# Optimization experiments

Hardware: AMD Instinct MI355X
Metric: run time of the kernel (lower is better)

The kernel has to match this reference:

```python
import jax, jax.numpy as jnp
import numpy as np

B, S, D, H, L, DFF, WIN = 2, 2048, 768, 12, 2, 3072, 512
EPS = 1e-5
DH = D // H


def setup_inputs() -> dict:
    key = jax.random.key(0)
    ks = jax.random.split(key, 8)
    rn = lambda k, shape: jax.random.normal(k, shape, jnp.float32) * 0.02
    inp = {
        "src": jax.random.normal(ks[0], (B, S, D), jnp.float32),
        "qw": rn(ks[1], (L, D, D)), "qb": jnp.zeros((L, D), jnp.float32),
        "kw": rn(ks[2], (L, D, D)), "kb": jnp.zeros((L, D), jnp.float32),
        "vw": rn(ks[3], (L, D, D)), "vb": jnp.zeros((L, D), jnp.float32),
        "ow": rn(ks[4], (L, D, D)), "ob": jnp.zeros((L, D), jnp.float32),
        "w1": rn(ks[5], (L, DFF, D)), "b1": jnp.zeros((L, DFF), jnp.float32),
        "w2": rn(ks[6], (L, D, DFF)), "b2": jnp.zeros((L, D), jnp.float32),
        "g1": jnp.ones((L, D), jnp.float32), "be1": jnp.zeros((L, D), jnp.float32),
        "g2": jnp.ones((L, D), jnp.float32), "be2": jnp.zeros((L, D), jnp.float32),
    }
    return inp


def _ln(x, g, b):
    m = jnp.mean(x, axis=-1, keepdims=True)
    v = jnp.mean(jnp.square(x - m), axis=-1, keepdims=True)
    return (x - m) * jax.lax.rsqrt(v + EPS) * g + b


def _encoder(src, qw, qb, kw, kb, vw, vb, ow, ob, w1, b1, w2, b2, g1, be1, g2, be2):
    scale = DH ** -0.5
    idx = jnp.arange(S)
    # non-causal sliding window: |i - j| <= window_size // 2
    band = jnp.abs(idx[:, None] - idx[None, :]) <= (WIN // 2)
    neg = -jnp.finfo(jnp.float32).max
    x = src
    for l in range(L):
        # projections -> (B, H, S, DH)
        q = (x @ qw[l].T + qb[l]).reshape(B, S, H, DH).transpose(0, 2, 1, 3)
        k = (x @ kw[l].T + kb[l]).reshape(B, S, H, DH).transpose(0, 2, 1, 3)
        v = (x @ vw[l].T + vb[l]).reshape(B, S, H, DH).transpose(0, 2, 1, 3)
        # full dense scores then band mask (faithful to the original module)
        sim = jnp.einsum('bhid,bhjd->bhij', q * scale, k)
        sim = jnp.where(band, sim, neg)
        attn = jax.nn.softmax(sim, axis=-1)
        o = jnp.einsum('bhij,bhjd->bhid', attn, v)
        o = o.transpose(0, 2, 1, 3).reshape(B, S, D) @ ow[l].T + ob[l]
        # post-norm transformer block (norm_first=False)
        x = _ln(x + o, g1[l], be1[l])
        ff = jax.nn.relu(x @ w1[l].T + b1[l]) @ w2[l].T + b2[l]
        x = _ln(x + ff, g2[l], be2[l])
    return x


def reference(src, qw, qb, kw, kb, vw, vb, ow, ob, w1, b1, w2, b2, g1, be1, g2, be2):
    return _encoder(src, qw, qb, kw, kb, vw, vb, ow, ob, w1, b1, w2, b2, g1, be1, g2, be2)
```

## Files before the change

### kernel.cpp

```cpp
#include <hip/hip_runtime.h>
#include <math.h>

#define BATCH 2
#define SEQ   2048
#define DM    768
#define NHD   12
#define NL    2
#define DFF   3072
#define DH    64
#define HW    256
#define MR    (BATCH*SEQ)
#define EPSF  1e-5f
#define SCALE 0.125f
#define QKVS  2304

typedef __attribute__((ext_vector_type(8))) __bf16 bf16x8;
typedef __attribute__((ext_vector_type(4))) float  f32x4;

__device__ __forceinline__ ushort f2bu(float f) {
    union { __bf16 h; ushort u; } c;
    c.h = (__bf16)f;
    return c.u;
}
__device__ __forceinline__ float bu2f(ushort u) {
    union { uint u; float f; } c;
    c.u = ((uint)u) << 16;
    return c.f;
}

__device__ __forceinline__ void gload16(const ushort* g, ushort* l) {
    __builtin_amdgcn_global_load_lds(
        (const __attribute__((address_space(1))) void*)g,
        (__attribute__((address_space(3))) void*)l, 16, 0, 0);
}

__device__ __forceinline__ void xcd_swz(int& bx, int& by, int& bz) {
    const int gx = gridDim.x, gy = gridDim.y;
    const int nwg = gx * gy * gridDim.z;
    int lin = bx + gx * (by + gy * bz);
    lin = (lin & 7) * (nwg >> 3) + (lin >> 3);
    bx = lin % gx;
    int rest = lin / gx;
    by = rest % gy;
    bz = rest / gy;
}

__global__ __launch_bounds__(256) void prep(
    const float* __restrict__ qw, const float* __restrict__ kw,
    const float* __restrict__ vw, const float* __restrict__ ow,
    const float* __restrict__ w1, const float* __restrict__ w2,
    const float* __restrict__ src,
    const float* __restrict__ qb, const float* __restrict__ kb,
    const float* __restrict__ vb,
    ushort* __restrict__ qkvwB, ushort* __restrict__ owB,
    ushort* __restrict__ w1B, ushort* __restrict__ w2B,
    ushort* __restrict__ xb, float* __restrict__ bcat)
{
    const int WD1C  = DM * DM;
    const int WQKVC = 3 * WD1C;
    const int WF1C  = DFF * DM;
    const int NB0 = NL * WQKVC / 1024;
    const int NB1 = NL * WD1C / 1024;
    const int NB2 = NL * WF1C / 1024;
    const int NB4 = MR * DM / 1024;

    int b = blockIdx.x;
    const int tid = threadIdx.x;

    if (b < NB0) {
        int e = b * 1024 + tid * 4;
        int l = e / WQKVC;
        int r = e % WQKVC;
        const float* s; int off;
        if (r < WD1C)          { s = qw + (size_t)l * WD1C; off = r; }
        else if (r < 2 * WD1C) { s = kw + (size_t)l * WD1C; off = r - WD1C; }
        else                   { s = vw + (size_t)l * WD1C; off = r - 2 * WD1C; }
        float4 v = *(const float4*)(s + off);
        ushort4 o4;
        o4.x = f2bu(v.x); o4.y = f2bu(v.y); o4.z = f2bu(v.z); o4.w = f2bu(v.w);
        *(ushort4*)(qkvwB + (size_t)l * WQKVC + r) = o4;
        return;
    }
    b -= NB0;
    if (b < NB1) {
        int i = b * 1024 + tid * 4;
        float4 v = *(const float4*)(ow + i);
        ushort4 o4;
        o4.x = f2bu(v.x); o4.y = f2bu(v.y); o4.z = f2bu(v.z); o4.w = f2bu(v.w);
        *(ushort4*)(owB + i) = o4;
        return;
    }
    b -= NB1;
    if (b < NB2) {
        int i = b * 1024 + tid * 4;
        float4 v = *(const float4*)(w1 + i);
        ushort4 o4;
        o4.x = f2bu(v.x); o4.y = f2bu(v.y); o4.z = f2bu(v.z); o4.w = f2bu(v.w);
        *(ushort4*)(w1B + i) = o4;
        return;
    }
    b -= NB2;
    if (b < NB2) {
        int i = b * 1024 + tid * 4;
        float4 v = *(const float4*)(w2 + i);
        ushort4 o4;
        o4.x = f2bu(v.x); o4.y = f2bu(v.y); o4.z = f2bu(v.z); o4.w = f2bu(v.w);
        *(ushort4*)(w2B + i) = o4;
        return;
    }
    b -= NB2;
    if (b < NB4) {
        int i = b * 1024 + tid * 4;
        float4 v = *(const float4*)(src + i);
        ushort4 o4;
        o4.x = f2bu(v.x); o4.y = f2bu(v.y); o4.z = f2bu(v.z); o4.w = f2bu(v.w);
        *(ushort4*)(xb + i) = o4;
        return;
    }
#pragma unroll
    for (int e = 0; e < 18; ++e) {
        int j = tid + 256 * e;
        int l = j / (3 * DM);
        int r = j % (3 * DM);
        int sel = r / DM, off = r % DM;
        const float* s = (sel == 0) ? qb : (sel == 1) ? kb : vb;
        bcat[(size_t)l * QKVS + sel * DM + off] = s[(size_t)l * DM + off];
    }
}

#define STAGE128(bi, kt) do {                                           \
        const int _k0 = (kt) * 32;                                      \
        gload16(ag + _k0,                    &As[bi][t * 8]);           \
        gload16(ag + (size_t)64 * ldk + _k0, &As[bi][2048 + t * 8]);    \
        gload16(wg + _k0,                    &Ws[bi][t * 8]);           \
        gload16(wg + (size_t)64 * ldk + _k0, &Ws[bi][2048 + t * 8]);    \
    } while (0)

__global__ __launch_bounds__(256) void gemm128(
    const ushort* __restrict__ A, const ushort* __restrict__ W,
    const float* __restrict__ bias, ushort* __restrict__ C,
    float* __restrict__ part, int M, int N, int Kc, int ldk, int relu)
{
    __shared__ ushort As[3][128 * 32];
    __shared__ ushort Ws[3][128 * 32];

    int bxi = blockIdx.x, byi = blockIdx.y, bzi = blockIdx.z;
    xcd_swz(bxi, byi, bzi);

    const int t  = threadIdx.x;
    const int bm = byi * 128;
    const int bn = bxi * 128;
    const int z  = bzi;
    const int kbase = z * Kc;

    const int w    = t >> 6;
    const int lane = t & 63;
    const int quad = lane >> 4;
    const int lrow = lane & 15;
    const int wm   = (w >> 1) * 64;
    const int wn   = (w & 1) * 64;
    const int rx   = (lrow >> 1) & 3;
    const int rq   = (quad ^ rx) * 8;

    const int srow = t >> 2;
    const int scol = (((t & 3) ^ ((t >> 3) & 3)) * 8);
    const ushort* ag = A + (size_t)(bm + srow) * ldk + kbase + scol;
    const ushort* wg = W + (size_t)(bn + srow) * ldk + kbase + scol;

    f32x4 acc[4][4] = {};
    const int NT = Kc / 32;

    STAGE128(0, 0);
    STAGE128(1, 1);

    for (int kt = 0; kt < NT; ++kt) {
        if (kt + 1 < NT)
            asm volatile("s_waitcnt vmcnt(4)" ::: "memory");
        else
            asm volatile("s_waitcnt vmcnt(0)" ::: "memory");
        __builtin_amdgcn_s_barrier();

        const int cb = kt % 3;
        bf16x8 af[4], bfr[4];
#pragma unroll
        for (int i = 0; i < 4; ++i)
            af[i] = *(const bf16x8*)&As[cb][(wm + i * 16 + lrow) * 32 + rq];
#pragma unroll
        for (int j = 0; j < 4; ++j)
            bfr[j] = *(const bf16x8*)&Ws[cb][(wn + j * 16 + lrow) * 32 + rq];

        __builtin_amdgcn_s_setprio(1);
#pragma unroll
        for (int i = 0; i < 4; ++i)
#pragma unroll
            for (int j = 0; j < 4; ++j)
                acc[i][j] = __builtin_amdgcn_mfma_f32_16x16x32_bf16(
                    af[i], bfr[j], acc[i][j], 0, 0, 0);
        __builtin_amdgcn_s_setprio(0);

        if (kt + 2 < NT) {
            const int sb = (kt + 2) % 3;
            STAGE128(sb, kt + 2);
        }
    }

    if (gridDim.z > 1) {
        float* po = part + (size_t)z * M * N;
#pragma unroll
        for (int j = 0; j < 4; ++j) {
            const int col = bn + wn + j * 16 + lrow;
#pragma unroll
            for (int i = 0; i < 4; ++i) {
                const int rb = bm + wm + i * 16 + quad * 4;
#pragma unroll
                for (int r = 0; r < 4; ++r)
                    po[(size_t)(rb + r) * N + col] = acc[i][j][r];
            }
        }
    } else {
#pragma unroll
        for (int j = 0; j < 4; ++j) {
            const int col = bn + wn + j * 16 + lrow;
            const float bv = bias[col];
#pragma unroll
            for (int i = 0; i < 4; ++i) {
                const int rb = bm + wm + i * 16 + quad * 4;
#pragma unroll
                for (int r = 0; r < 4; ++r) {
                    float vv = acc[i][j][r] + bv;
                    if (relu) vv = fmaxf(vv, 0.f);
                    C[(size_t)(rb + r) * N + col] = f2bu(vv);
                }
            }
        }
    }
}

#define STAGE64(bi, kt) do {                                            \
        const int _k0 = (kt) * 32;                                      \
        gload16(ag + _k0,                    &As[bi][t * 8]);           \
        gload16(wg + _k0,                    &Ws[bi][t * 8]);           \
        gload16(wg + (size_t)64 * ldk + _k0, &Ws[bi][2048 + t * 8]);    \
    } while (0)

__global__ __launch_bounds__(256) void gemm64(
    const ushort* __restrict__ A, const ushort* __restrict__ W,
    const float* __restrict__ bias, ushort* __restrict__ C,
    float* __restrict__ part, int M, int N, int Kc, int ldk, int relu)
{
    __shared__ ushort As[3][64 * 32];
    __shared__ ushort Ws[3][128 * 32];

    int bxi = blockIdx.x, byi = blockIdx.y, bzi = blockIdx.z;
    xcd_swz(bxi, byi, bzi);

    const int t  = threadIdx.x;
    const int bm = byi * 64;
    const int bn = bxi * 128;
    const int z  = bzi;
    const int kbase = z * Kc;

    const int w    = t >> 6;
    const int lane = t & 63;
    const int quad = lane >> 4;
    const int lrow = lane & 15;
    const int wm   = (w >> 1) * 32;
    const int wn   = (w & 1) * 64;
    const int rx   = (lrow >> 1) & 3;
    const int rq   = (quad ^ rx) * 8;

    const int srow = t >> 2;
    const int scol = (((t & 3) ^ ((t >> 3) & 3)) * 8);
    const ushort* ag = A + (size_t)(bm + srow) * ldk + kbase + scol;
    const ushort* wg = W + (size_t)(bn + srow) * ldk + kbase + scol;

    f32x4 acc[2][4] = {};
    const int NT = Kc / 32;

    STAGE64(0, 0);
    STAGE64(1, 1);

    for (int kt = 0; kt < NT; ++kt) {
        if (kt + 1 < NT)
            asm volatile("s_waitcnt vmcnt(3)" ::: "memory");
        else
            asm volatile("s_waitcnt vmcnt(0)" ::: "memory");
        __builtin_amdgcn_s_barrier();

        const int cb = kt % 3;
        bf16x8 af[2], bfr[4];
#pragma unroll
        for (int i = 0; i < 2; ++i)
            af[i] = *(const bf16x8*)&As[cb][(wm + i * 16 + lrow) * 32 + rq];
#pragma unroll
        for (int j = 0; j < 4; ++j)
            bfr[j] = *(const bf16x8*)&Ws[cb][(wn + j * 16 + lrow) * 32 + rq];

        __builtin_amdgcn_s_setprio(1);
#pragma unroll
        for (int i = 0; i < 2; ++i)
#pragma unroll
            for (int j = 0; j < 4; ++j)
                acc[i][j] = __builtin_amdgcn_mfma_f32_16x16x32_bf16(
                    af[i], bfr[j], acc[i][j], 0, 0, 0);
        __builtin_amdgcn_s_setprio(0);

        if (kt + 2 < NT) {
            const int sb = (kt + 2) % 3;
            STAGE64(sb, kt + 2);
        }
    }

    if (gridDim.z > 1) {
        float* po = part + (size_t)z * M * N;
#pragma unroll
        for (int j = 0; j < 4; ++j) {
            const int col = bn + wn + j * 16 + lrow;
#pragma unroll
            for (int i = 0; i < 2; ++i) {
                const int rb = bm + wm + i * 16 + quad * 4;
#pragma unroll
                for (int r = 0; r < 4; ++r)
                    po[(size_t)(rb + r) * N + col] = acc[i][j][r];
            }
        }
    } else {
#pragma unroll
        for (int j = 0; j < 4; ++j) {
            const int col = bn + wn + j * 16 + lrow;
            const float bv = bias[col];
#pragma unroll
            for (int i = 0; i < 2; ++i) {
                const int rb = bm + wm + i * 16 + quad * 4;
#pragma unroll
                for (int r = 0; r < 4; ++r) {
                    float vv = acc[i][j][r] + bv;
                    if (relu) vv = fmaxf(vv, 0.f);
                    C[(size_t)(rb + r) * N + col] = f2bu(vv);
                }
            }
        }
    }
}

#define QT  128
#define NCH 10
#define KP  72

__global__ __launch_bounds__(512) void attn(
    const ushort* __restrict__ q, const ushort* __restrict__ k,
    const ushort* __restrict__ v, ushort* __restrict__ o)
{
    __shared__ ushort kv[2][64][KP];
    __shared__ ushort vt[2][64][KP];
    __shared__ ushort sc[QT][KP];

    int bxi = blockIdx.x, byi = blockIdx.y, bzi = blockIdx.z;
    xcd_swz(bxi, byi, bzi);

    const int t    = threadIdx.x;
    const int i0   = bxi * QT;
    const int h    = byi;
    const int b    = bzi;
    const size_t ibase = (size_t)b * SEQ * QKVS + (size_t)h * DH;
    const size_t obase = (size_t)b * SEQ * DM   + (size_t)h * DH;

    const int w    = t >> 6;
    const int lane = t & 63;
    const int quad = lane >> 4;
    const int lrow = lane & 15;
    const int qrow = w * 16;

    const int jstart = i0 - HW;
    const int clo = (qrow + 78) >> 6;
    const int chi = (qrow + 449) >> 6;

    const int sjj = t >> 3;
    const int sd0 = (t & 7) * 8;

#pragma unroll
    for (int e = 0; e < 2; ++e) {
        int idx = t + 512 * e;
        int qi = idx >> 3, d0 = (idx & 7) * 8;
        uint4 raw = *(const uint4*)(q + ibase + (size_t)(i0 + qi) * QKVS + d0);
        *(uint4*)&sc[qi][d0] = raw;
    }
    uint4 kr, vr;
    {
        int j = jstart + sjj;
        kr = make_uint4(0, 0, 0, 0);
        vr = make_uint4(0, 0, 0, 0);
        if (j >= 0 && j < SEQ) {
            kr = *(const uint4*)(k + ibase + (size_t)j * QKVS + sd0);
            vr = *(const uint4*)(v + ibase + (size_t)j * QKVS + sd0);
        }
    }
    *(uint4*)&kv[0][sjj][sd0] = kr;
    {
        const ushort* u = (const ushort*)&vr;
#pragma unroll
        for (int x = 0; x < 8; ++x) {
            int dh  = sd0 + x;
            int blk = ((sjj >> 3) ^ (dh >> 3)) & 7;
            vt[0][dh][blk * 8 + (sjj & 7)] = u[x];
        }
    }
    __syncthreads();

    const bf16x8 a0 = *(const bf16x8*)&sc[qrow + lrow][quad * 8];
    const bf16x8 a1 = *(const bf16x8*)&sc[qrow + lrow][32 + quad * 8];

    float m_s = -1e20f, l_s = 0.f;
    f32x4 oacc[4] = {};

    for (int c = 0; c < NCH; ++c) {
        const int cur = c & 1;
        const int j0  = jstart + c * 64;

        if (c + 1 < NCH) {
            int j = jstart + (c + 1) * 64 + sjj;
            kr = make_uint4(0, 0, 0, 0);
            vr = make_uint4(0, 0, 0, 0);
            if (j >= 0 && j < SEQ) {
                kr = *(const uint4*)(k + ibase + (size_t)j * QKVS + sd0);
                vr = *(const uint4*)(v + ibase + (size_t)j * QKVS + sd0);
            }
        }

        const bool full = (c >= clo) && (c <= chi) &&
                          (j0 >= 0) && (j0 + 64 <= SEQ);
        float p[4][4];
#pragma unroll
        for (int kt = 0; kt < 4; ++kt) {
            const int krow = kt * 16;
            bf16x8 kf0 = *(const bf16x8*)&kv[cur][krow + lrow][quad * 8];
            bf16x8 kf1 = *(const bf16x8*)&kv[cur][krow + lrow][32 + quad * 8];
            f32x4 acc = {};
            __builtin_amdgcn_s_setprio(1);
            acc = __builtin_amdgcn_mfma_f32_16x16x32_bf16(kf0, a0, acc, 0, 0, 0);
            acc = __builtin_amdgcn_mfma_f32_16x16x32_bf16(kf1, a1, acc, 0, 0, 0);
            __builtin_amdgcn_s_setprio(0);
            if (full) {
#pragma unroll
                for (int r = 0; r < 4; ++r) p[kt][r] = acc[r] * SCALE;
            } else {
                const int ig = i0 + qrow + lrow;
#pragma unroll
                for (int r = 0; r < 4; ++r) {
                    const int jg = j0 + krow + quad * 4 + r;
                    bool ok = (jg >= 0) && (jg < SEQ) &&
                              (jg >= ig - HW) && (jg <= ig + HW);
                    p[kt][r] = ok ? acc[r] * SCALE : -1e30f;
                }
            }
        }

        float cm = p[0][0];
#pragma unroll
        for (int kt = 0; kt < 4; ++kt)
#pragma unroll
            for (int r = 0; r < 4; ++r) cm = fmaxf(cm, p[kt][r]);
        cm = fmaxf(cm, __shfl_xor(cm, 16));
        cm = fmaxf(cm, __shfl_xor(cm, 32));

        const bool resc = !__all(cm <= m_s + 8.f);
        float f = 1.f;
        if (resc) {
            const float mn = fmaxf(m_s, cm);
            f = __expf(m_s - mn);
            m_s = mn;
        }
        float cs = 0.f;
#pragma unroll
        for (int kt = 0; kt < 4; ++kt)
#pragma unroll
            for (int r = 0; r < 4; ++r) {
                float e = __expf(p[kt][r] - m_s);
                p[kt][r] = e;
                cs += e;
            }
        cs += __shfl_xor(cs, 16);
        cs += __shfl_xor(cs, 32);
        l_s = l_s * f + cs;
        if (resc) {
            float f4[4];
#pragma unroll
            for (int r = 0; r < 4; ++r) f4[r] = __shfl(f, quad * 4 + r);
#pragma unroll
            for (int nt = 0; nt < 4; ++nt)
#pragma unroll
                for (int r = 0; r < 4; ++r) oacc[nt][r] *= f4[r];
        }

#pragma unroll
        for (int kt = 0; kt < 4; ++kt) {
            ushort4 pw;
            pw.x = f2bu(p[kt][0]);
            pw.y = f2bu(p[kt][1]);
            pw.z = f2bu(p[kt][2]);
            pw.w = f2bu(p[kt][3]);
            *(ushort4*)&sc[qrow + lrow][kt * 16 + quad * 4] = pw;
        }

        bf16x8 pa0 = *(const bf16x8*)&sc[qrow + lrow][quad * 8];
        bf16x8 pa1 = *(const bf16x8*)&sc[qrow + lrow][32 + quad * 8];
        __builtin_amdgcn_s_setprio(1);
#pragma unroll
        for (int nt = 0; nt < 4; ++nt) {
            const int dh  = nt * 16 + lrow;
            const int rsw = (dh >> 3) & 7;
            bf16x8 b0 = *(const bf16x8*)&vt[cur][dh][((quad)     ^ rsw) * 8];
            bf16x8 b1 = *(const bf16x8*)&vt[cur][dh][((quad + 4) ^ rsw) * 8];
            oacc[nt] = __builtin_amdgcn_mfma_f32_16x16x32_bf16(pa0, b0, oacc[nt], 0, 0, 0);
            oacc[nt] = __builtin_amdgcn_mfma_f32_16x16x32_bf16(pa1, b1, oacc[nt], 0, 0, 0);
        }
        __builtin_amdgcn_s_setprio(0);

        if (c + 1 < NCH) {
            const int nxt = cur ^ 1;
            *(uint4*)&kv[nxt][sjj][sd0] = kr;
            const ushort* u = (const ushort*)&vr;
#pragma unroll
            for (int x = 0; x < 8; ++x) {
                int dh  = sd0 + x;
                int blk = ((sjj >> 3) ^ (dh >> 3)) & 7;
                vt[nxt][dh][blk * 8 + (sjj & 7)] = u[x];
            }
        }
        __syncthreads();
    }

    const float inv = 1.f / l_s;
    float inv4[4];
#pragma unroll
    for (int r = 0; r < 4; ++r) inv4[r] = __shfl(inv, quad * 4 + r);
#pragma unroll
    for (int r = 0; r < 4; ++r) {
        const int qi = i0 + qrow + quad * 4 + r;
#pragma unroll
        for (int nt = 0; nt < 4; ++nt)
            o[obase + (size_t)qi * DM + nt * 16 + lrow] = f2bu(oacc[nt][r] * inv4[r]);
    }
}

__global__ __launch_bounds__(256) void add_ln_sk(
    const ushort* __restrict__ xa, const float* __restrict__ pp,
    const float* __restrict__ bias, const float* __restrict__ g,
    const float* __restrict__ be,
    ushort* __restrict__ ob, float* __restrict__ of, int fin)
{
    const int r = blockIdx.x * 4 + (threadIdx.x >> 6);
    const int t = threadIdx.x & 63;
    const size_t off = (size_t)r * DM;
    const size_t pl  = (size_t)MR * DM;
    float sv[12];
    float s1 = 0.f, s2 = 0.f;
#pragma unroll
    for (int ii = 0; ii < 12; ++ii) {
        const int c = t + 64 * ii;
        float vv = bu2f(xa[off + c]) + pp[off + c] + pp[pl + off + c] + bias[c];
        sv[ii] = vv; s1 += vv; s2 += vv * vv;
    }
#pragma unroll
    for (int o2 = 32; o2; o2 >>= 1) {
        s1 += __shfl_xor(s1, o2);
        s2 += __shfl_xor(s2, o2);
    }
    const float mean = s1 * (1.f / 768.f);
    const float rstd = rsqrtf(s2 * (1.f / 768.f) - mean * mean + EPSF);
#pragma unroll
    for (int ii = 0; ii < 12; ++ii) {
        const int c = t + 64 * ii;
        float v = (sv[ii] - mean) * rstd * g[c] + be[c];
        if (fin) of[off + c] = v;
        else     ob[off + c] = f2bu(v);
    }
}

__global__ __launch_bounds__(256) void add_ln_sk3(
    const ushort* __restrict__ xa, const float* __restrict__ pp,
    const float* __restrict__ bias, const float* __restrict__ g,
    const float* __restrict__ be,
    ushort* __restrict__ ob, float* __restrict__ of, int fin)
{
    const int r = blockIdx.x * 4 + (threadIdx.x >> 6);
    const int t = threadIdx.x & 63;
    const size_t off = (size_t)r * DM;
    const size_t pl  = (size_t)MR * DM;
    float sv[12];
    float s1 = 0.f, s2 = 0.f;
#pragma unroll
    for (int ii = 0; ii < 12; ++ii) {
        const int c = t + 64 * ii;
        float vv = bu2f(xa[off + c]) + pp[off + c] + pp[pl + off + c]
                 + pp[2 * pl + off + c] + bias[c];
        sv[ii] = vv; s1 += vv; s2 += vv * vv;
    }
#pragma unroll
    for (int o2 = 32; o2; o2 >>= 1) {
        s1 += __shfl_xor(s1, o2);
        s2 += __shfl_xor(s2, o2);
    }
    const float mean = s1 * (1.f / 768.f);
    const float rstd = rsqrtf(s2 * (1.f / 768.f) - mean * mean + EPSF);
#pragma unroll
    for (int ii = 0; ii < 12; ++ii) {
        const int c = t + 64 * ii;
        float v = (sv[ii] - mean) * rstd * g[c] + be[c];
        if (fin) of[off + c] = v;
        else     ob[off + c] = f2bu(v);
    }
}

extern "C" void kernel_launch(void* const* d_in, const int* in_sizes, int n_in,
                              void* d_out, int out_size, void* d_ws, size_t ws_size,
                              hipStream_t stream) {
    (void)in_sizes; (void)n_in; (void)out_size; (void)ws_size;
    const float* src = (const float*)d_in[0];
    const float* qw  = (const float*)d_in[1];
    const float* qb  = (const float*)d_in[2];
    const float* kw  = (const float*)d_in[3];
    const float* kb  = (const float*)d_in[4];
    const float* vw  = (const float*)d_in[5];
    const float* vb  = (const float*)d_in[6];
    const float* ow  = (const float*)d_in[7];
    const float* ob  = (const float*)d_in[8];
    const float* w1  = (const float*)d_in[9];
    const float* b1  = (const float*)d_in[10];
    const float* w2  = (const float*)d_in[11];
    const float* b2  = (const float*)d_in[12];
    const float* g1  = (const float*)d_in[13];
    const float* be1 = (const float*)d_in[14];
    const float* g2  = (const float*)d_in[15];
    const float* be2 = (const float*)d_in[16];

    const size_t A    = (size_t)MR * DM;
    const size_t WD1  = (size_t)DM * DM;
    const size_t WQKV = (size_t)3 * DM * DM;
    const size_t WF1  = (size_t)DFF * DM;
    const size_t WF   = (size_t)NL * WF1;

    float*  bcat = (float*)d_ws;
    ushort* p    = (ushort*)(bcat + (size_t)NL * QKVS);
    ushort* qkvwB = p; p += (size_t)NL * WQKV;
    ushort* owB   = p; p += (size_t)NL * WD1;
    ushort* w1B   = p; p += WF;
    ushort* w2B   = p; p += WF;
    ushort* xb    = p; p += A;
    ushort* qkvB  = p; p += 3 * A;
    ushort* oB    = p; p += A;
    ushort* yB    = p; p += A;
    ushort* h1    = p; p += A;
    ushort* ffh   = p; p += 4 * A;
    ushort* x2    = p;

    float* partF = (float*)xb;
    float* partO = (float*)ffh;

    const int PB = (int)((NL * WQKV + NL * WD1 + 2 * WF + A) / 1024) + 1;
    prep<<<PB, 256, 0, stream>>>(qw, kw, vw, ow, w1, w2, src,
                                 qb, kb, vb,
                                 qkvwB, owB, w1B, w2B, xb, bcat);

    const dim3 gQKV(QKVS / 128, MR / 128);
    const dim3 gOp(DM / 128, MR / 64, 2);
    const dim3 gF1(DFF / 128, MR / 128);
    const dim3 gF2(DM / 128, MR / 128, 3);
    const dim3 gA(SEQ / QT, NHD, BATCH);

    for (int l = 0; l < NL; ++l) {
        const size_t bD = (size_t)l * DM;
        const size_t bF = (size_t)l * DFF;
        const ushort* xin = (l == 0) ? xb : x2;

        gemm128<<<gQKV, 256, 0, stream>>>(xin, qkvwB + (size_t)l * WQKV,
                                          bcat + (size_t)l * QKVS, qkvB,
                                          nullptr, MR, QKVS, DM, DM, 0);
        attn<<<gA, 512, 0, stream>>>(qkvB, qkvB + DM, qkvB + 2 * DM, oB);
        gemm64<<<gOp, 256, 0, stream>>>(oB, owB + (size_t)l * WD1, nullptr,
                                        nullptr, partO, MR, DM, DM / 2, DM, 0);
        add_ln_sk<<<MR / 4, 256, 0, stream>>>(xin, partO, ob + bD,
                                              g1 + bD, be1 + bD,
                                              h1, nullptr, 0);
        gemm128<<<gF1, 256, 0, stream>>>(h1, w1B + (size_t)l * WF1, b1 + bF, ffh,
                                         nullptr, MR, DFF, DM, DM, 1);
        gemm128<<<gF2, 256, 0, stream>>>(ffh, w2B + (size_t)l * WF1, nullptr,
                                         nullptr, partF, MR, DM, DFF / 3, DFF, 0);
        if (l == NL - 1)
            add_ln_sk3<<<MR / 4, 256, 0, stream>>>(h1, partF, b2 + bD,
                                                   g2 + bD, be2 + bD,
                                                   nullptr, (float*)d_out, 1);
        else
            add_ln_sk3<<<MR / 4, 256, 0, stream>>>(h1, partF, b2 + bD,
                                                   g2 + bD, be2 + bD,
                                                   x2, nullptr, 0);
    }
}
```

Before: 432.3 us.

## Stage GEMM epilogue through LDS and shrink attention query tile to 64

```diff
diff --git a/kernel.cpp b/kernel.cpp
--- a/kernel.cpp
+++ b/kernel.cpp
@@ -128,12 +128,12 @@
     }
 }
 
-#define STAGE128(bi, kt) do {                                           \
-        const int _k0 = (kt) * 32;                                      \
-        gload16(ag + _k0,                    &As[bi][t * 8]);           \
-        gload16(ag + (size_t)64 * ldk + _k0, &As[bi][2048 + t * 8]);    \
-        gload16(wg + _k0,                    &Ws[bi][t * 8]);           \
-        gload16(wg + (size_t)64 * ldk + _k0, &Ws[bi][2048 + t * 8]);    \
+#define STAGE128(bi, kt) do {                                             \
+        const int _k0 = (kt) * 32;                                        \
+        gload16(ag + _k0,                    As + (bi)*4096 + t * 8);     \
+        gload16(ag + (size_t)64 * ldk + _k0, As + (bi)*4096 + 2048 + t * 8); \
+        gload16(wg + _k0,                    Ws + (bi)*4096 + t * 8);     \
+        gload16(wg + (size_t)64 * ldk + _k0, Ws + (bi)*4096 + 2048 + t * 8); \
     } while (0)
 
 __global__ __launch_bounds__(256) void gemm128(
@@ -141,8 +141,9 @@
     const float* __restrict__ bias, ushort* __restrict__ C,
     float* __restrict__ part, int M, int N, int Kc, int ldk, int relu)
 {
-    __shared__ ushort As[3][128 * 32];
-    __shared__ ushort Ws[3][128 * 32];
+    __shared__ ushort smem[24576];
+    ushort* const As = smem;
+    ushort* const Ws = smem + 12288;
 
     int bxi = blockIdx.x, byi = blockIdx.y, bzi = blockIdx.z;
     xcd_swz(bxi, byi, bzi);
@@ -184,10 +185,10 @@
         bf16x8 af[4], bfr[4];
 #pragma unroll
         for (int i = 0; i < 4; ++i)
-            af[i] = *(const bf16x8*)&As[cb][(wm + i * 16 + lrow) * 32 + rq];
+            af[i] = *(const bf16x8*)&As[cb * 4096 + (wm + i * 16 + lrow) * 32 + rq];
 #pragma unroll
         for (int j = 0; j < 4; ++j)
-            bfr[j] = *(const bf16x8*)&Ws[cb][(wn + j * 16 + lrow) * 32 + rq];
+            bfr[j] = *(const bf16x8*)&Ws[cb * 4096 + (wn + j * 16 + lrow) * 32 + rq];
 
         __builtin_amdgcn_s_setprio(1);
 #pragma unroll
@@ -218,20 +219,29 @@
             }
         }
     } else {
+        ushort* lc = smem;
+        __syncthreads();
 #pragma unroll
         for (int j = 0; j < 4; ++j) {
-            const int col = bn + wn + j * 16 + lrow;
-            const float bv = bias[col];
+            const int col = wn + j * 16 + lrow;
+            const float bv = bias[bn + col];
 #pragma unroll
             for (int i = 0; i < 4; ++i) {
-                const int rb = bm + wm + i * 16 + quad * 4;
+                const int rb = wm + i * 16 + quad * 4;
 #pragma unroll
                 for (int r = 0; r < 4; ++r) {
                     float vv = acc[i][j][r] + bv;
                     if (relu) vv = fmaxf(vv, 0.f);
-                    C[(size_t)(rb + r) * N + col] = f2bu(vv);
+                    lc[(rb + r) * 128 + col] = f2bu(vv);
                 }
             }
+        }
+        __syncthreads();
+#pragma unroll
+        for (int e = 0; e < 8; ++e) {
+            int idx = e * 2048 + t * 8;
+            int row = idx >> 7, col = idx & 127;
+            *(uint4*)(C + (size_t)(bm + row) * N + bn + col) = *(uint4*)&lc[idx];
         }
     }
 }
@@ -343,11 +353,11 @@
     }
 }
 
-#define QT  128
-#define NCH 10
+#define QT  64
+#define NCH 9
 #define KP  72
 
-__global__ __launch_bounds__(512) void attn(
+__global__ __launch_bounds__(256) void attn(
     const ushort* __restrict__ q, const ushort* __restrict__ k,
     const ushort* __restrict__ v, ushort* __restrict__ o)
 {
@@ -372,37 +382,37 @@
     const int qrow = w * 16;
 
     const int jstart = i0 - HW;
-    const int clo = (qrow + 78) >> 6;
-    const int chi = (qrow + 449) >> 6;
-
-    const int sjj = t >> 3;
+
+    const int sjj[2] = { t >> 3, (t + 256) >> 3 };
     const int sd0 = (t & 7) * 8;
 
 #pragma unroll
     for (int e = 0; e < 2; ++e) {
-        int idx = t + 512 * e;
+        int idx = t + 256 * e;
         int qi = idx >> 3, d0 = (idx & 7) * 8;
         uint4 raw = *(const uint4*)(q + ibase + (size_t)(i0 + qi) * QKVS + d0);
         *(uint4*)&sc[qi][d0] = raw;
     }
-    uint4 kr, vr;
-    {
-        int j = jstart + sjj;
-        kr = make_uint4(0, 0, 0, 0);
-        vr = make_uint4(0, 0, 0, 0);
+    uint4 kr[2], vr[2];
+#pragma unroll
+    for (int e = 0; e < 2; ++e) {
+        int j = jstart + sjj[e];
+        kr[e] = make_uint4(0, 0, 0, 0);
+        vr[e] = make_uint4(0, 0, 0, 0);
         if (j >= 0 && j < SEQ) {
-            kr = *(const uint4*)(k + ibase + (size_t)j * QKVS + sd0);
-            vr = *(const uint4*)(v + ibase + (size_t)j * QKVS + sd0);
-        }
-    }
-    *(uint4*)&kv[0][sjj][sd0] = kr;
-    {
-        const ushort* u = (const ushort*)&vr;
+            kr[e] = *(const uint4*)(k + ibase + (size_t)j * QKVS + sd0);
+            vr[e] = *(const uint4*)(v + ibase + (size_t)j * QKVS + sd0);
+        }
+    }
+#pragma unroll
+    for (int e = 0; e < 2; ++e) {
+        *(uint4*)&kv[0][sjj[e]][sd0] = kr[e];
+        const ushort* u = (const ushort*)&vr[e];
 #pragma unroll
         for (int x = 0; x < 8; ++x) {
             int dh  = sd0 + x;
-            int blk = ((sjj >> 3) ^ (dh >> 3)) & 7;
-            vt[0][dh][blk * 8 + (sjj & 7)] = u[x];
+            int blk = ((sjj[e] >> 3) ^ (dh >> 3)) & 7;
+            vt[0][dh][blk * 8 + (sjj[e] & 7)] = u[x];
         }
     }
     __syncthreads();
@@ -418,17 +428,20 @@
         const int j0  = jstart + c * 64;
 
         if (c + 1 < NCH) {
-            int j = jstart + (c + 1) * 64 + sjj;
-            kr = make_uint4(0, 0, 0, 0);
-            vr = make_uint4(0, 0, 0, 0);
-            if (j >= 0 && j < SEQ) {
-                kr = *(const uint4*)(k + ibase + (size_t)j * QKVS + sd0);
-                vr = *(const uint4*)(v + ibase + (size_t)j * QKVS + sd0);
+            const int j0n = jstart + (c + 1) * 64;
+#pragma unroll
+            for (int e = 0; e < 2; ++e) {
+                int j = j0n + sjj[e];
+                kr[e] = make_uint4(0, 0, 0, 0);
+                vr[e] = make_uint4(0, 0, 0, 0);
+                if (j >= 0 && j < SEQ) {
+                    kr[e] = *(const uint4*)(k + ibase + (size_t)j * QKVS + sd0);
+                    vr[e] = *(const uint4*)(v + ibase + (size_t)j * QKVS + sd0);
+                }
             }
         }
 
-        const bool full = (c >= clo) && (c <= chi) &&
-                          (j0 >= 0) && (j0 + 64 <= SEQ);
+        const bool full = (c >= 1) && (c <= 7) && (j0 >= 0) && (j0 + 64 <= SEQ);
         float p[4][4];
 #pragma unroll
         for (int kt = 0; kt < 4; ++kt) {
@@ -518,13 +531,16 @@
 
         if (c + 1 < NCH) {
             const int nxt = cur ^ 1;
-            *(uint4*)&kv[nxt][sjj][sd0] = kr;
-            const ushort* u = (const ushort*)&vr;
-#pragma unroll
-            for (int x = 0; x < 8; ++x) {
-                int dh  = sd0 + x;
-                int blk = ((sjj >> 3) ^ (dh >> 3)) & 7;
-                vt[nxt][dh][blk * 8 + (sjj & 7)] = u[x];
+#pragma unroll
+            for (int e = 0; e < 2; ++e) {
+                *(uint4*)&kv[nxt][sjj[e]][sd0] = kr[e];
+                const ushort* u = (const ushort*)&vr[e];
+#pragma unroll
+                for (int x = 0; x < 8; ++x) {
+                    int dh  = sd0 + x;
+                    int blk = ((sjj[e] >> 3) ^ (dh >> 3)) & 7;
+                    vt[nxt][dh][blk * 8 + (sjj[e] & 7)] = u[x];
+                }
             }
         }
         __syncthreads();
@@ -676,7 +692,7 @@
         gemm128<<<gQKV, 256, 0, stream>>>(xin, qkvwB + (size_t)l * WQKV,
                                           bcat + (size_t)l * QKVS, qkvB,
                                           nullptr, MR, QKVS, DM, DM, 0);
-        attn<<<gA, 512, 0, stream>>>(qkvB, qkvB + DM, qkvB + 2 * DM, oB);
+        attn<<<gA, 256, 0, stream>>>(qkvB, qkvB + DM, qkvB + 2 * DM, oB);
         gemm64<<<gOp, 256, 0, stream>>>(oB, owB + (size_t)l * WD1, nullptr,
                                         nullptr, partO, MR, DM, DM / 2, DM, 0);
         add_ln_sk<<<MR / 4, 256, 0, stream>>>(xin, partO, ob + bD,
```

New measurement: 439.0 us. No clear change (+1.5%).
